# Performance work log

Hardware: AMD Instinct MI355X
Metric: run time of the kernel (lower is better)

Reference implementation:

```python
import jax, jax.numpy as jnp
import numpy as np

N1, N2 = 8192, 8192
E1, E2 = 131072, 131072
F_IN, NH, B = 64, 128, 256
D6 = 6 * NH  # set2set in_channels = 768


def _gcn(x, W, b, src, dst, ew, n):
    xw = x @ W
    loop = jnp.arange(n)
    s = jnp.concatenate([src, loop])
    d = jnp.concatenate([dst, loop])
    w = jnp.concatenate([ew, jnp.ones((n,), ew.dtype)])
    deg = jax.ops.segment_sum(w, d, num_segments=n)
    dinv = jnp.where(deg > 0, jax.lax.rsqrt(deg), 0.0)
    norm = (dinv[s] * w * dinv[d])[:, None]
    return jax.ops.segment_sum(xw[s] * norm, d, num_segments=n) + b


def _leaky(x):
    return jax.nn.leaky_relu(x, 0.2)


def _l2norm(x):
    return x / jnp.maximum(jnp.linalg.norm(x, axis=1, keepdims=True), 1e-12)


def _set2set(x, batch, nseg, Wih, Whh, bih, bhh, steps=2):
    # Set2Set pooling: LSTM(input=2d, hidden=d) + segment softmax attention
    d = x.shape[1]
    h = jnp.zeros((nseg, d), x.dtype)
    c = jnp.zeros((nseg, d), x.dtype)
    q_star = jnp.zeros((nseg, 2 * d), x.dtype)
    for _ in range(steps):
        gates = q_star @ Wih.T + h @ Whh.T + bih + bhh
        gi, gf, gg, go = jnp.split(gates, 4, axis=1)  # torch LSTM gate order i,f,g,o
        c = jax.nn.sigmoid(gf) * c + jax.nn.sigmoid(gi) * jnp.tanh(gg)
        h = jax.nn.sigmoid(go) * jnp.tanh(c)
        e = jnp.sum(x * h[batch], axis=1)
        emax = jax.ops.segment_max(e, batch, num_segments=nseg)
        ee = jnp.exp(e - emax[batch])
        a = ee / jax.ops.segment_sum(ee, batch, num_segments=nseg)[batch]
        r = jax.ops.segment_sum(a[:, None] * x, batch, num_segments=nseg)
        q_star = jnp.concatenate([h, r], axis=1)
    return q_star


def setup_inputs():
    key = jax.random.key(0)
    ks = jax.random.split(key, 20)
    f32 = jnp.float32

    def xav(k, shp):
        fan_in, fan_out = shp[-1], shp[0] if len(shp) == 2 else shp[-1]
        lim = float(np.sqrt(6.0 / (shp[0] + shp[1])))
        return jax.random.uniform(k, shp, f32, -lim, lim)

    inp = {}
    inp["features_1"] = jax.random.normal(ks[0], (N1, F_IN), f32)
    inp["features_2"] = jax.random.normal(ks[1], (N2, F_IN), f32)
    inp["edge_attr_1"] = jax.random.uniform(ks[2], (E1,), f32)
    inp["edge_attr_2"] = jax.random.uniform(ks[3], (E2,), f32)
    inp["W0"] = xav(ks[4], (F_IN, NH)); inp["b0"] = jnp.zeros((NH,), f32)
    inp["W1"] = xav(ks[5], (NH, NH)); inp["b1"] = jnp.zeros((NH,), f32)
    inp["W2"] = xav(ks[6], (NH, NH)); inp["b2"] = jnp.zeros((NH,), f32)
    inp["Wih"] = xav(ks[7], (4 * D6, 2 * D6)); inp["bih"] = jnp.zeros((4 * D6,), f32)
    inp["Whh"] = xav(ks[8], (4 * D6, D6)); inp["bhh"] = jnp.zeros((4 * D6,), f32)
    inp["Wp1"] = xav(ks[9], (256, 4 * D6)); inp["bp1"] = jnp.zeros((256,), f32)
    inp["Wp2"] = xav(ks[10], (128, 256)); inp["bp2"] = jnp.zeros((128,), f32)
    inp["Wp3"] = xav(ks[11], (1, 128)); inp["bp3"] = jnp.zeros((1,), f32)
    inp["edge_index_1"] = jax.random.randint(ks[12], (2, E1), 0, N1)
    inp["edge_index_2"] = jax.random.randint(ks[13], (2, E2), 0, N2)
    inp["batch_1"] = jnp.sort(jax.random.randint(ks[14], (N1,), 0, B))
    inp["batch_2"] = jnp.sort(jax.random.randint(ks[15], (N2,), 0, B))
    return inp


def reference(features_1, features_2, edge_attr_1, edge_attr_2,
              W0, b0, W1, b1, W2, b2, Wih, bih, Whh, bhh,
              Wp1, bp1, Wp2, bp2, Wp3, bp3,
              edge_index_1, edge_index_2, batch_1, batch_2):
    s1, d1 = edge_index_1[0], edge_index_1[1]
    s2, d2 = edge_index_2[0], edge_index_2[1]

    f1a = _leaky(_gcn(features_1, W0, b0, s1, d1, edge_attr_1, N1))
    f2a = _leaky(_gcn(features_2, W0, b0, s2, d2, edge_attr_2, N2))
    f1b = _leaky(_gcn(f1a, W1, b1, s1, d1, edge_attr_1, N1))
    f2b = _leaky(_gcn(f2a, W1, b1, s2, d2, edge_attr_2, N2))
    f1c = _leaky(_gcn(f1b, W2, b2, s1, d1, edge_attr_1, N1))
    f2c = _leaky(_gcn(f2b, W2, b2, s2, d2, edge_attr_2, N2))
    h1 = jnp.concatenate([f1a, f1b, f1c], axis=1)  # [N1, 3*NH]
    h2 = jnp.concatenate([f2a, f2b, f2c], axis=1)  # [N2, 3*NH]

    # interaction: cosine-sim map masked to same-graph pairs (len_map)
    ns = _l2norm(h1)
    nv = _l2norm(h2)
    mask = (batch_1[:, None] == batch_2[None, :]).astype(ns.dtype)  # [N1, N2]
    imap = (ns @ nv.T) * mask
    f1 = jnp.concatenate([ns, imap @ nv], axis=1)      # [N1, 6*NH]
    f2 = jnp.concatenate([nv, imap.T @ ns], axis=1)    # [N2, 6*NH]

    g1 = _set2set(f1, batch_1, B, Wih, Whh, bih, bhh)  # [B, 12*NH]
    g2 = _set2set(f2, batch_2, B, Wih, Whh, bih, bhh)  # [B, 12*NH]
    z = jnp.concatenate([g1, g2], axis=1)              # [B, 24*NH]
    z = jax.nn.relu(z @ Wp1.T + bp1)
    z = jax.nn.relu(z @ Wp2.T + bp2)
    z = z @ Wp3.T + bp3
    return jax.nn.sigmoid(z).reshape(-1)
```

## Files before the change

### kernel.cpp

```cpp
#include <hip/hip_runtime.h>
#include <cmath>

#define N_NODES 8192
#define N_EDGES 131072
#define NB      256
#define NH      128
#define D3      384
#define D6      768
#define SMM     96
#define SLD     104
#define MAXDEG  64

typedef __attribute__((ext_vector_type(8))) short short8v;
typedef __attribute__((ext_vector_type(4))) float f32x4;
typedef unsigned short bf16t;

__device__ __forceinline__ float sigf(float x){ return 1.0f/(1.0f+__expf(-x)); }
__device__ __forceinline__ unsigned short f2bf(float x){
  unsigned u = __float_as_uint(x);
  unsigned r = u + 0x7FFF + ((u>>16)&1);
  return (unsigned short)(r>>16);
}
__device__ __forceinline__ float bfl(unsigned u){ return __uint_as_float(u<<16); }
__device__ __forceinline__ float bfh(unsigned u){ return __uint_as_float(u & 0xFFFF0000u); }
__device__ __forceinline__ float b2f(bf16t u){ return __uint_as_float(((unsigned)u)<<16); }
__device__ __forceinline__ float h0val(const float* bih, const float* bhh, int j){
  float c = sigf(bih[j]+bhh[j]) * tanhf(bih[2*D6+j]+bhh[2*D6+j]);
  return sigf(bih[3*D6+j]+bhh[3*D6+j]) * tanhf(c);
}

__device__ __forceinline__ void xw_body(int vb, int t,
    const bf16t* __restrict__ x1, const bf16t* __restrict__ x2, int xs, int K,
    const bf16t* __restrict__ Wt, bf16t* __restrict__ xw1, bf16t* __restrict__ xw2){
  int side = vb >> 8; int b = vb & 255;
  const bf16t* x = side? x2:x1;
  bf16t* xw = side? xw2:xw1;
  int w = t>>6, lane = t&63;
  int lm = lane&15, quad = lane>>4;
  int r0 = b*32 + (w>>1)*16;
  int c0 = (w&1)*64;
  const bf16t* a = x + (size_t)(r0+lm)*xs + quad*8;
  f32x4 acc[4] = {};
  for (int k=0;k<K;k+=32){
    short8v af = *(const short8v*)(a + k);
    #pragma unroll
    for (int ni=0;ni<4;ni++){
      short8v bf = *(const short8v*)(Wt + (size_t)(c0+ni*16+lm)*K + quad*8 + k);
      acc[ni] = __builtin_amdgcn_mfma_f32_16x16x32_bf16(af, bf, acc[ni], 0,0,0);
    }
  }
  #pragma unroll
  for (int ni=0;ni<4;ni++)
    #pragma unroll
    for (int r=0;r<4;r++){
      int row = r0 + quad*4 + r, col = c0 + ni*16 + lm;
      xw[(size_t)row*NH + col] = f2bf(acc[ni][r]);
    }
}


__global__ __launch_bounds__(256) void k_setup(
    const float* __restrict__ fe1, const float* __restrict__ fe2,
    short* __restrict__ xf1, short* __restrict__ xf2,
    const float* __restrict__ W0, const float* __restrict__ W1, const float* __restrict__ W2,
    bf16t* __restrict__ Wt,
    int* ecur1, int* ecur2, int* cnt1, int* cnt2){
  int b = blockIdx.x, tid = threadIdx.x;
  if (b < 1024){
    int t = b*256 + tid;
    int side = t >= 131072; int i = t & 131071;
    float4 v = ((const float4*)(side? fe2:fe1))[i];
    short4 o = { (short)f2bf(v.x), (short)f2bf(v.y), (short)f2bf(v.z), (short)f2bf(v.w) };
    ((short4*)(side? xf2:xf1))[i] = o;
  } else if (b < 1027){
    int l = b - 1024;
    const float* W = (l==0)? W0 : ((l==1)? W1 : W2);
    int K = (l==0)? 64 : 128;
    bf16t* dst = Wt + ((l==0)? 0 : ((l==1)? 128*64 : 128*64+128*128));
    for (int idx = tid; idx < 128*K; idx += 256){
      int n = idx / K, k = idx - n*K;
      dst[idx] = f2bf(W[k*NH + n]);
    }
  } else {
    int t = (b-1027)*256 + tid;
    if (t < N_NODES){ ecur1[t]=0; ecur2[t]=0; }
    if (t < NB){ cnt1[t]=0; cnt2[t]=0; }
  }
}

__global__ __launch_bounds__(256) void k_fill2(
    const int* __restrict__ ei1, const float* __restrict__ ea1,
    const int* __restrict__ ei2, const float* __restrict__ ea2,
    int* cur1, int* es1, float* ec1, int* cur2, int* es2, float* ec2,
    const int* __restrict__ b1, const int* __restrict__ b2, int* cnt1, int* cnt2,
    const bf16t* __restrict__ xf1, const bf16t* __restrict__ xf2,
    const bf16t* __restrict__ Wt, bf16t* __restrict__ xwA1, bf16t* __restrict__ xwA2){
  int blk = blockIdx.x;
  if (blk < 1024){
    int idx = blk*256 + threadIdx.x;
    int side = idx >= N_EDGES;
    int e = idx & (N_EDGES-1);
    const int* ei = side? ei2:ei1; const float* ea = side? ea2:ea1;
    int* cur = side? cur2:cur1; int* es = side? es2:es1; float* ec = side? ec2:ec1;
    int s = ei[e], d = ei[N_EDGES+e];
    int pos = atomicAdd(&cur[d], 1);
    if (pos < MAXDEG){
      es[d*MAXDEG + pos] = s;
      ec[d*MAXDEG + pos] = ea[e];
    }
    if (idx < N_NODES){ atomicAdd(&cnt1[b1[idx]],1); atomicAdd(&cnt2[b2[idx]],1); }
  } else {
    xw_body(blk-1024, threadIdx.x, xf1, xf2, 64, 64, Wt, xwA1, xwA2);
  }
}

__global__ __launch_bounds__(256) void k_deg2(
    const int* __restrict__ cur1, const float* __restrict__ ec1, float* deg1,
    const int* __restrict__ cur2, const float* __restrict__ ec2, float* deg2,
    const int* __restrict__ c1, const int* __restrict__ c2, int* st1, int* st2){
  __shared__ int ps[256];
  int blk = blockIdx.x, t = threadIdx.x;
  if (blk < 64){
    int idx = blk*256 + t;
    int side = idx >= N_NODES;
    int i = idx & (N_NODES-1);
    const int* cur = side? cur2:cur1;
    const float* ec = side? ec2:ec1;
    float* deg = side? deg2:deg1;
    int ce = cur[i]; if (ce > MAXDEG) ce = MAXDEG;
    float s = 1.0f;
    const float* p = ec + (size_t)i*MAXDEG;
    for (int k=0;k<ce;k++) s += p[k];
    deg[i] = s;
  } else {
    const int* c = (blk==65)? c2:c1; int* st = (blk==65)? st2:st1;
    ps[t]=c[t]; __syncthreads();
    for (int d=1; d<256; d<<=1){
      int v = (t>=d)? ps[t-d]:0;
      __syncthreads();
      ps[t]+=v;
      __syncthreads();
    }
    st[t+1]=ps[t];
    if (t==0) st[0]=0;
  }
}


__global__ __launch_bounds__(256) void k_gxw(
    const bf16t* __restrict__ xwi1, const bf16t* __restrict__ xwi2,
    const int* __restrict__ cur1, const int* __restrict__ cur2,
    const int* __restrict__ es1, const int* __restrict__ es2,
    float* __restrict__ ec1, float* __restrict__ ec2,
    const float* __restrict__ d1, const float* __restrict__ d2,
    const float* __restrict__ bias, int loff, int coefmode,
    bf16t* __restrict__ h1, bf16t* __restrict__ h2,
    const bf16t* __restrict__ Wl,
    bf16t* __restrict__ xwo1, bf16t* __restrict__ xwo2){
  int blk = blockIdx.x;
  int side = blk >> 9; int b = blk & 511;
  const ushort4* xw = (const ushort4*)(side? xwi2:xwi1);
  const int* cur = side? cur2:cur1;
  const int* es  = side? es2:es1;
  float* ec = side? ec2:ec1;
  const float* deg = side? d2:d1;
  bf16t* h = side? h2:h1;
  int t = threadIdx.x;
  int c4 = t & 31;
  float4 bv = ((const float4*)bias)[c4];
  #pragma unroll
  for (int grp=0; grp<2; grp++){
    int i = b*16 + grp*8 + (t>>5);
    float dgi = deg[i];
    float sc = 1.0f/dgi;
    float rsq_d = rsqrtf(dgi);
    ushort4 v = xw[(size_t)i*32 + c4];
    float4 acc = {b2f(v.x)*sc, b2f(v.y)*sc, b2f(v.z)*sc, b2f(v.w)*sc};
    int r = i*MAXDEG;
    int ce = cur[i]; if (ce > MAXDEG) ce = MAXDEG;
    int r1 = r + ce;
    for (; r+3<r1; r+=4){
      int s0=es[r], s1=es[r+1], s2=es[r+2], s3=es[r+3];
      float w0=ec[r], w1=ec[r+1], w2=ec[r+2], w3=ec[r+3];
      if (coefmode){
        w0 *= rsqrtf(deg[s0])*rsq_d;
        w1 *= rsqrtf(deg[s1])*rsq_d;
        w2 *= rsqrtf(deg[s2])*rsq_d;
        w3 *= rsqrtf(deg[s3])*rsq_d;
        if (c4==0){ ec[r]=w0; ec[r+1]=w1; ec[r+2]=w2; ec[r+3]=w3; }
      }
      ushort4 u0 = xw[(size_t)s0*32 + c4];
      ushort4 u1 = xw[(size_t)s1*32 + c4];
      ushort4 u2 = xw[(size_t)s2*32 + c4];
      ushort4 u3 = xw[(size_t)s3*32 + c4];
      acc.x += b2f(u0.x)*w0 + b2f(u1.x)*w1 + b2f(u2.x)*w2 + b2f(u3.x)*w3;
      acc.y += b2f(u0.y)*w0 + b2f(u1.y)*w1 + b2f(u2.y)*w2 + b2f(u3.y)*w3;
      acc.z += b2f(u0.z)*w0 + b2f(u1.z)*w1 + b2f(u2.z)*w2 + b2f(u3.z)*w3;
      acc.w += b2f(u0.w)*w0 + b2f(u1.w)*w1 + b2f(u2.w)*w2 + b2f(u3.w)*w3;
    }
    for (; r<r1; r++){
      int s0=es[r]; float w0=ec[r];
      if (coefmode){
        w0 *= rsqrtf(deg[s0])*rsq_d;
        if (c4==0) ec[r]=w0;
      }
      ushort4 u0 = xw[(size_t)s0*32 + c4];
      acc.x+=b2f(u0.x)*w0; acc.y+=b2f(u0.y)*w0; acc.z+=b2f(u0.z)*w0; acc.w+=b2f(u0.w)*w0;
    }
    acc.x+=bv.x; acc.y+=bv.y; acc.z+=bv.z; acc.w+=bv.w;
    acc.x = (acc.x>0.f)?acc.x:0.2f*acc.x;
    acc.y = (acc.y>0.f)?acc.y:0.2f*acc.y;
    acc.z = (acc.z>0.f)?acc.z:0.2f*acc.z;
    acc.w = (acc.w>0.f)?acc.w:0.2f*acc.w;
    ((ushort4*)(h + (size_t)i*D3 + loff))[c4] =
      make_ushort4(f2bf(acc.x), f2bf(acc.y), f2bf(acc.z), f2bf(acc.w));
  }
  __syncthreads();
  int w = t>>6, lane = t&63;
  int lm = lane&15, quad = lane>>4;
  const bf16t* x = (side? h2:h1) + loff;
  int r0 = b*16;
  int c0 = w*32;
  const bf16t* a = x + (size_t)(r0+lm)*D3 + quad*8;
  bf16t* xwo = side? xwo2:xwo1;
  f32x4 acc0={0,0,0,0}, acc1={0,0,0,0};
  for (int k=0;k<128;k+=32){
    short8v af = *(const short8v*)(a + k);
    short8v b0 = *(const short8v*)(Wl + (size_t)(c0+lm)*128 + quad*8 + k);
    short8v b1 = *(const short8v*)(Wl + (size_t)(c0+16+lm)*128 + quad*8 + k);
    acc0 = __builtin_amdgcn_mfma_f32_16x16x32_bf16(af, b0, acc0, 0,0,0);
    acc1 = __builtin_amdgcn_mfma_f32_16x16x32_bf16(af, b1, acc1, 0,0,0);
  }
  #pragma unroll
  for (int r=0;r<4;r++){
    int row = r0 + quad*4 + r;
    xwo[(size_t)row*NH + c0 + lm]      = f2bf(acc0[r]);
    xwo[(size_t)row*NH + c0 + 16 + lm] = f2bf(acc1[r]);
  }
}

__global__ __launch_bounds__(256) void k_gather(const bf16t* __restrict__ xw1, const bf16t* __restrict__ xw2,
                                                const int* __restrict__ cur1, const int* __restrict__ cur2,
                                                const int* __restrict__ es1, const int* __restrict__ es2,
                                                const float* __restrict__ ec1, const float* __restrict__ ec2,
                                                const float* __restrict__ d1, const float* __restrict__ d2,
                                                const float* __restrict__ b,
                                                bf16t* __restrict__ h1, bf16t* __restrict__ h2, int loff,
                                                int l2mode, bf16t* __restrict__ f1, bf16t* __restrict__ f2,
                                                const float* __restrict__ Wih, short* __restrict__ Wih16,
                                                const float* __restrict__ Wp1, short* __restrict__ Wp116,
                                                const float* __restrict__ Whh,
                                                const float* __restrict__ bih, const float* __restrict__ bhh,
                                                float* __restrict__ cvec){
  __shared__ float hs_cv[D6];
  int blk = blockIdx.x;
  int t = threadIdx.x;
  if (blk >= 2048){
    if (blk < 4352){
      int tt = (blk-2048)*256 + t;
      int n = tt/192, q = tt - n*192;
      float4 v = ((const float4*)(Wih + (size_t)n*1536 + 768))[q];
      short4 o = { (short)f2bf(v.x), (short)f2bf(v.y), (short)f2bf(v.z), (short)f2bf(v.w) };
      ((short4*)Wih16)[tt] = o;
    } else if (blk < 5120){
      int tt = (blk-4352)*256 + t;
      float4 v = ((const float4*)Wp1)[tt];
      short4 o = { (short)f2bf(v.x), (short)f2bf(v.y), (short)f2bf(v.z), (short)f2bf(v.w) };
      ((short4*)Wp116)[tt] = o;
    } else {
      int j0 = (blk - 5120)*4;
      for (int k=t; k<D6; k+=256) hs_cv[k] = h0val(bih,bhh,k);
      __syncthreads();
      int w = t>>6, lane = t&63;
      int j = j0 + w;
      const float4* wi = (const float4*)(Wih + (size_t)j*(2*D6));
      const float4* wh = (const float4*)(Whh + (size_t)j*D6);
      const float4* h4 = (const float4*)hs_cv;
      float acc=0;
      #pragma unroll
      for (int m=0;m<3;m++){
        float4 hv = h4[m*64+lane];
        float4 a = wi[m*64+lane];
        float4 bb = wh[m*64+lane];
        acc += hv.x*(a.x+bb.x) + hv.y*(a.y+bb.y) + hv.z*(a.z+bb.z) + hv.w*(a.w+bb.w);
      }
      #pragma unroll
      for (int m=1;m<64;m<<=1) acc += __shfl_xor(acc,m,64);
      if (lane==0) cvec[j]=acc+bih[j]+bhh[j];
    }
    return;
  }
  int side = blk >> 10; int bb = blk & 1023;
  const ushort4* xw = (const ushort4*)(side? xw2:xw1);
  const int* cur = side? cur2:cur1;
  const int* es  = side? es2:es1;
  const float* ec= side? ec2:ec1;
  const float* deg = side? d2:d1;
  bf16t* h = side? h2:h1;
  int i = bb*8 + (t>>5);
  int c4 = t & 31;
  float sc = 1.0f/deg[i];
  ushort4 v = xw[(size_t)i*32 + c4];
  float4 acc = {b2f(v.x)*sc, b2f(v.y)*sc, b2f(v.z)*sc, b2f(v.w)*sc};
  int r = i*MAXDEG;
  int ce = cur[i]; if (ce > MAXDEG) ce = MAXDEG;
  int r1 = r + ce;
  for (; r+3<r1; r+=4){
    int s0=es[r], s1=es[r+1], s2=es[r+2], s3=es[r+3];
    float w0=ec[r], w1=ec[r+1], w2=ec[r+2], w3=ec[r+3];
    ushort4 u0 = xw[(size_t)s0*32 + c4];
    ushort4 u1 = xw[(size_t)s1*32 + c4];
    ushort4 u2 = xw[(size_t)s2*32 + c4];
    ushort4 u3 = xw[(size_t)s3*32 + c4];
    acc.x += b2f(u0.x)*w0 + b2f(u1.x)*w1 + b2f(u2.x)*w2 + b2f(u3.x)*w3;
    acc.y += b2f(u0.y)*w0 + b2f(u1.y)*w1 + b2f(u2.y)*w2 + b2f(u3.y)*w3;
    acc.z += b2f(u0.z)*w0 + b2f(u1.z)*w1 + b2f(u2.z)*w2 + b2f(u3.z)*w3;
    acc.w += b2f(u0.w)*w0 + b2f(u1.w)*w1 + b2f(u2.w)*w2 + b2f(u3.w)*w3;
  }
  for (; r<r1; r++){
    int s0=es[r]; float w0=ec[r];
    ushort4 u0 = xw[(size_t)s0*32 + c4];
    acc.x+=b2f(u0.x)*w0; acc.y+=b2f(u0.y)*w0; acc.z+=b2f(u0.z)*w0; acc.w+=b2f(u0.w)*w0;
  }
  float4 bv = ((const float4*)b)[c4];
  acc.x+=bv.x; acc.y+=bv.y; acc.z+=bv.z; acc.w+=bv.w;
  acc.x = (acc.x>0.f)?acc.x:0.2f*acc.x;
  acc.y = (acc.y>0.f)?acc.y:0.2f*acc.y;
  acc.z = (acc.z>0.f)?acc.z:0.2f*acc.z;
  acc.w = (acc.w>0.f)?acc.w:0.2f*acc.w;
  if (!l2mode){
    ((ushort4*)(h + (size_t)i*D3 + loff))[c4] =
      make_ushort4(f2bf(acc.x), f2bf(acc.y), f2bf(acc.z), f2bf(acc.w));
  } else {
    ushort4 u0 = ((const ushort4*)(h + (size_t)i*D3))[c4];
    ushort4 u1 = ((const ushort4*)(h + (size_t)i*D3 + 128))[c4];
    float4 v0 = {b2f(u0.x), b2f(u0.y), b2f(u0.z), b2f(u0.w)};
    float4 v1 = {b2f(u1.x), b2f(u1.y), b2f(u1.z), b2f(u1.w)};
    float ss = v0.x*v0.x+v0.y*v0.y+v0.z*v0.z+v0.w*v0.w
             + v1.x*v1.x+v1.y*v1.y+v1.z*v1.z+v1.w*v1.w
             + acc.x*acc.x+acc.y*acc.y+acc.z*acc.z+acc.w*acc.w;
    #pragma unroll
    for (int m=1;m<32;m<<=1) ss += __shfl_xor(ss, m, 64);
    float scale = 1.0f/fmaxf(sqrtf(ss), 1e-12f);
    bf16t* f = side? f2:f1;
    ((ushort4*)(f + (size_t)i*D6))[c4]       = make_ushort4(f2bf(v0.x*scale),f2bf(v0.y*scale),f2bf(v0.z*scale),f2bf(v0.w*scale));
    ((ushort4*)(f + (size_t)i*D6 + 128))[c4] = make_ushort4(f2bf(v1.x*scale),f2bf(v1.y*scale),f2bf(v1.z*scale),f2bf(v1.w*scale));
    ((ushort4*)(f + (size_t)i*D6 + 256))[c4] = make_ushort4(f2bf(acc.x*scale),f2bf(acc.y*scale),f2bf(acc.z*scale),f2bf(acc.w*scale));
  }
}

__global__ __launch_bounds__(256) void k_inter(bf16t* __restrict__ f1, bf16t* __restrict__ f2,
                                               const int* __restrict__ st1, const int* __restrict__ st2,
                                               const float* __restrict__ bih, const float* __restrict__ bhh,
                                               bf16t* __restrict__ Ab){
  __shared__ __align__(16) bf16t Sld[SMM*SLD];
  int bx = blockIdx.x;
  int t = threadIdx.x;
  int side = bx >> 8, g = bx & (NB-1);
  int i0 = st1[g]; int n1 = st1[g+1]-i0; if (n1>SMM) n1=SMM;
  int j0 = st2[g]; int n2 = st2[g+1]-j0; if (n2>SMM) n2=SMM;
  int cnt = side? n2 : n1;
  int J   = side? n1 : n2;
  int r0base = side? j0 : i0;
  int c0base = side? i0 : j0;
  const bf16t* rowp = (side? f2 : f1);
  const bf16t* colp = (side? f1 : f2);
  const bf16t* src = colp + (size_t)c0base*D6;
  bf16t* dst = (side? f2 : f1) + (size_t)r0base*D6 + D3;
  int w = t>>6, lane = t&63;
  int lm = lane & 15, quad = lane >> 4;
  int nti = (cnt+15)>>4, ntj = (J+15)>>4;
  for (int tile = w; tile < nti*ntj; tile += 4){
    int ti = tile/ntj, tj = tile - ti*ntj;
    int ar = r0base + ti*16 + lm; if (ar > N_NODES-1) ar = N_NODES-1;
    int br = c0base + tj*16 + lm; if (br > N_NODES-1) br = N_NODES-1;
    const bf16t* a = rowp + (size_t)ar*D6 + quad*8;
    const bf16t* b = colp + (size_t)br*D6 + quad*8;
    f32x4 acc = {0,0,0,0};
    #pragma unroll
    for (int k=0; k<384; k+=32){
      short8v af = *(const short8v*)(a + k);
      short8v bf = *(const short8v*)(b + k);
      acc = __builtin_amdgcn_mfma_f32_16x16x32_bf16(af, bf, acc, 0, 0, 0);
    }
    int col = tj*16 + lm;
    #pragma unroll
    for (int r=0;r<4;r++){
      int row = ti*16 + quad*4 + r;
      if (row < cnt && col < J)
        Sld[row*SLD + col] = f2bf(acc[r]);
    }
  }
  __syncthreads();
  for (int row = w; row < cnt; row += 4){
    float acc[6] = {};
    const bf16t* sr = Sld + row*SLD;
    for (int j = 0; j < J; j++){
      float s = b2f(sr[j]);
      const uint* xr = (const uint*)(src + (size_t)j*D6);
      #pragma unroll
      for (int m=0;m<3;m++){
        uint rv = xr[m*64+lane];
        acc[m*2+0] += s*bfl(rv);
        acc[m*2+1] += s*bfh(rv);
      }
    }
    #pragma unroll
    for (int m=0;m<3;m++)
      ((ushort2*)(dst + (size_t)row*D6 + m*128))[lane] =
        make_ushort2(f2bf(acc[m*2]), f2bf(acc[m*2+1]));
  }
  __syncthreads();
  {
    float4* hs = (float4*)Sld;
    float* e_s = ((float*)Sld) + 768;
    float* part = ((float*)Sld) + 864;
    const bf16t* x = rowp + (size_t)r0base*D6;
    if (t<192){
      int j = t*4;
      hs[t] = make_float4(h0val(bih,bhh,j), h0val(bih,bhh,j+1), h0val(bih,bhh,j+2), h0val(bih,bhh,j+3));
    }
    __syncthreads();
    for (int n=w; n<cnt; n+=4){
      const uint2* xr = (const uint2*)(x + (size_t)n*D6);
      float p = 0;
      #pragma unroll
      for (int m=0;m<3;m++){
        uint2 rv = xr[m*64+lane];
        float4 hvv = hs[m*64+lane];
        p += bfl(rv.x)*hvv.x + bfh(rv.x)*hvv.y + bfl(rv.y)*hvv.z + bfh(rv.y)*hvv.w;
      }
      #pragma unroll
      for (int m=1;m<64;m<<=1) p += __shfl_xor(p,m,64);
      if (lane==0) e_s[n]=p;
    }
    __syncthreads();
    if (w==0){
      float mx=-INFINITY;
      for (int n=lane;n<cnt;n+=64) mx=fmaxf(mx,e_s[n]);
      #pragma unroll
      for (int m=1;m<64;m<<=1) mx=fmaxf(mx,__shfl_xor(mx,m,64));
      float s=0;
      for (int n=lane;n<cnt;n+=64) s+=__expf(e_s[n]-mx);
      #pragma unroll
      for (int m=1;m<64;m<<=1) s+=__shfl_xor(s,m,64);
      float inv=1.0f/s;
      for (int n=lane;n<cnt;n+=64) e_s[n]=__expf(e_s[n]-mx)*inv;
    }
    __syncthreads();
    float av[3][4] = {};
    for (int n=w; n<cnt; n+=4){
      float a = e_s[n];
      const uint2* xr = (const uint2*)(x + (size_t)n*D6);
      #pragma unroll
      for (int m=0;m<3;m++){
        uint2 rv = xr[m*64+lane];
        av[m][0]+=a*bfl(rv.x); av[m][1]+=a*bfh(rv.x); av[m][2]+=a*bfl(rv.y); av[m][3]+=a*bfh(rv.y);
      }
    }
    #pragma unroll
    for (int m=0;m<3;m++)
      *(float4*)&part[w*D6 + (m*64+lane)*4] = make_float4(av[m][0],av[m][1],av[m][2],av[m][3]);
    __syncthreads();
    if (t<192){
      float4 p0 = *(const float4*)&part[0*D6 + t*4];
      float4 p1 = *(const float4*)&part[1*D6 + t*4];
      float4 p2 = *(const float4*)&part[2*D6 + t*4];
      float4 p3 = *(const float4*)&part[3*D6 + t*4];
      float4 s = make_float4(p0.x+p1.x+p2.x+p3.x, p0.y+p1.y+p2.y+p3.y,
                             p0.z+p1.z+p2.z+p3.z, p0.w+p1.w+p2.w+p3.w);
      ushort4 o = make_ushort4(f2bf(s.x), f2bf(s.y), f2bf(s.z), f2bf(s.w));
      ((ushort4*)(Ab + (size_t)(side*NB+g)*D6))[t]=o;
    }
  }
}


__global__ __launch_bounds__(256) void k_att(const bf16t* __restrict__ f1, const bf16t* __restrict__ f2,
                                             const float* __restrict__ hbase, int perseg,
                                             const float* __restrict__ bih, const float* __restrict__ bhh,
                                             const int* __restrict__ st1, const int* __restrict__ st2,
                                             bf16t* __restrict__ dst16, long sidestep, long dstride){
  __shared__ float4 hs[192];
  __shared__ float e_s[SMM];
  __shared__ float part[4][D6];
  int side = blockIdx.x >> 8, g = blockIdx.x & (NB-1);
  const int* st = side? st2:st1;
  int n0 = st[g]; int cnt = st[g+1]-n0; if (cnt>SMM) cnt=SMM;
  const bf16t* x = (side? f2:f1) + (size_t)n0*D6;
  int t = threadIdx.x, w = t>>6, lane = t&63;
  if (t<192){
    if (perseg){
      hs[t] = ((const float4*)(hbase + (size_t)(side*NB+g)*D6))[t];
    } else {
      int j = t*4;
      hs[t] = make_float4(h0val(bih,bhh,j), h0val(bih,bhh,j+1), h0val(bih,bhh,j+2), h0val(bih,bhh,j+3));
    }
  }
  __syncthreads();
  for (int n=w; n<cnt; n+=4){
    const uint2* xr = (const uint2*)(x + (size_t)n*D6);
    float p = 0;
    #pragma unroll
    for (int m=0;m<3;m++){
      uint2 rv = xr[m*64+lane];
      float4 hvv = hs[m*64+lane];
      p += bfl(rv.x)*hvv.x + bfh(rv.x)*hvv.y + bfl(rv.y)*hvv.z + bfh(rv.y)*hvv.w;
    }
    #pragma unroll
    for (int m=1;m<64;m<<=1) p += __shfl_xor(p,m,64);
    if (lane==0) e_s[n]=p;
  }
  __syncthreads();
  if (w==0){
    float mx=-INFINITY;
    for (int n=lane;n<cnt;n+=64) mx=fmaxf(mx,e_s[n]);
    #pragma unroll
    for (int m=1;m<64;m<<=1) mx=fmaxf(mx,__shfl_xor(mx,m,64));
    float s=0;
    for (int n=lane;n<cnt;n+=64) s+=__expf(e_s[n]-mx);
    #pragma unroll
    for (int m=1;m<64;m<<=1) s+=__shfl_xor(s,m,64);
    float inv=1.0f/s;
    for (int n=lane;n<cnt;n+=64) e_s[n]=__expf(e_s[n]-mx)*inv;
  }
  __syncthreads();
  float av[3][4] = {};
  for (int n=w; n<cnt; n+=4){
    float a = e_s[n];
    const uint2* xr = (const uint2*)(x + (size_t)n*D6);
    #pragma unroll
    for (int m=0;m<3;m++){
      uint2 rv = xr[m*64+lane];
      av[m][0]+=a*bfl(rv.x); av[m][1]+=a*bfh(rv.x); av[m][2]+=a*bfl(rv.y); av[m][3]+=a*bfh(rv.y);
    }
  }
  #pragma unroll
  for (int m=0;m<3;m++)
    *(float4*)&part[w][(m*64+lane)*4] = make_float4(av[m][0],av[m][1],av[m][2],av[m][3]);
  __syncthreads();
  if (t<192){
    float4 p0 = *(const float4*)&part[0][t*4];
    float4 p1 = *(const float4*)&part[1][t*4];
    float4 p2 = *(const float4*)&part[2][t*4];
    float4 p3 = *(const float4*)&part[3][t*4];
    float4 s = make_float4(p0.x+p1.x+p2.x+p3.x, p0.y+p1.y+p2.y+p3.y,
                           p0.z+p1.z+p2.z+p3.z, p0.w+p1.w+p2.w+p3.w);
    ushort4 o = make_ushort4(f2bf(s.x), f2bf(s.y), f2bf(s.z), f2bf(s.w));
    ushort4* dp = (ushort4*)(dst16 + side*sidestep + (size_t)g*dstride);
    dp[t]=o;
  }
}

__global__ __launch_bounds__(256) void k_gates(const short* __restrict__ A16,
                                               const short* __restrict__ B16,
                                               const float* __restrict__ cvec,
                                               const float* __restrict__ bih, const float* __restrict__ bhh,
                                               float* __restrict__ h1s, bf16t* __restrict__ z16){
  __shared__ float gbuf[4][16][66];
  int w = threadIdx.x >> 6, lane = threadIdx.x & 63;
  int lm = lane & 15, quad = lane >> 4;
  int bm = blockIdx.x * 16;
  int jb = blockIdx.y * 64;
  const short* a = A16 + (size_t)(bm + lm)*768 + quad*8;
  const short* b = B16 + (size_t)(w*768 + jb + lm)*768 + quad*8;
  f32x4 acc0={0,0,0,0}, acc1={0,0,0,0}, acc2={0,0,0,0}, acc3={0,0,0,0};
  for (int k=0; k<768; k+=32){
    short8v af = *(const short8v*)(a + k);
    short8v b0 = *(const short8v*)(b + k);
    short8v b1 = *(const short8v*)(b + 16*768 + k);
    short8v b2 = *(const short8v*)(b + 32*768 + k);
    short8v b3 = *(const short8v*)(b + 48*768 + k);
    acc0 = __builtin_amdgcn_mfma_f32_16x16x32_bf16(af, b0, acc0, 0, 0, 0);
    acc1 = __builtin_amdgcn_mfma_f32_16x16x32_bf16(af, b1, acc1, 0, 0, 0);
    acc2 = __builtin_amdgcn_mfma_f32_16x16x32_bf16(af, b2, acc2, 0, 0, 0);
    acc3 = __builtin_amdgcn_mfma_f32_16x16x32_bf16(af, b3, acc3, 0, 0, 0);
  }
  #pragma unroll
  for (int r=0;r<4;r++){
    gbuf[w][quad*4+r][lm]      = acc0[r];
    gbuf[w][quad*4+r][16+lm]   = acc1[r];
    gbuf[w][quad*4+r][32+lm]   = acc2[r];
    gbuf[w][quad*4+r][48+lm]   = acc3[r];
  }
  __syncthreads();
  int t = threadIdx.x;
  #pragma unroll
  for (int u=0; u<4; u++){
    int p = t + u*256;
    int mm = p>>6, jj = p&63;
    int j = jb + jj, m = bm + mm;
    float g4[4];
    #pragma unroll
    for (int q=0;q<4;q++) g4[q] = gbuf[q][mm][jj] + cvec[q*D6 + j];
    float c0j = sigf(bih[j]+bhh[j]) * tanhf(bih[2*D6+j]+bhh[2*D6+j]);
    float c = sigf(g4[1])*c0j + sigf(g4[0])*tanhf(g4[2]);
    float h = sigf(g4[3])*tanhf(c);
    h1s[(size_t)m*D6 + j] = h;
    int side = m>>8, g = m&255;
    z16[(size_t)g*3072 + side*1536 + j] = f2bf(h);
  }
}

__global__ __launch_bounds__(256) void k_gemm_mfma_p1(const short* __restrict__ A16,
                                                      const short* __restrict__ B16,
                                                      float* __restrict__ pout){
  int w = threadIdx.x >> 6, lane = threadIdx.x & 63;
  int lm = lane & 15, quad = lane >> 4;
  int bm = blockIdx.x * 16;
  int bn = w * 64;
  int kbase = blockIdx.y * 192;
  const short* a = A16 + (size_t)(bm + lm)*3072 + quad*8 + kbase;
  const short* b = B16 + (size_t)(bn + lm)*3072 + quad*8 + kbase;
  f32x4 acc0={0,0,0,0}, acc1={0,0,0,0}, acc2={0,0,0,0}, acc3={0,0,0,0};
  for (int k=0; k<192; k+=32){
    short8v af = *(const short8v*)(a + k);
    short8v b0 = *(const short8v*)(b + k);
    short8v b1 = *(const short8v*)(b + 16*3072 + k);
    short8v b2 = *(const short8v*)(b + 32*3072 + k);
    short8v b3 = *(const short8v*)(b + 48*3072 + k);
    acc0 = __builtin_amdgcn_mfma_f32_16x16x32_bf16(af, b0, acc0, 0, 0, 0);
    acc1 = __builtin_amdgcn_mfma_f32_16x16x32_bf16(af, b1, acc1, 0, 0, 0);
    acc2 = __builtin_amdgcn_mfma_f32_16x16x32_bf16(af, b2, acc2, 0, 0, 0);
    acc3 = __builtin_amdgcn_mfma_f32_16x16x32_bf16(af, b3, acc3, 0, 0, 0);
  }
  float* po = pout + (size_t)blockIdx.y*256*256;
  #pragma unroll
  for (int r=0;r<4;r++){
    size_t base = (size_t)(bm + quad*4 + r)*256 + bn + lm;
    po[base]      = acc0[r];
    po[base + 16] = acc1[r];
    po[base + 32] = acc2[r];
    po[base + 48] = acc3[r];
  }
}

__global__ __launch_bounds__(128) void k_p23(const float* __restrict__ pbuf, const float* __restrict__ bp1,
                                             const float* __restrict__ Wp2, const float* __restrict__ bp2,
                                             const float* __restrict__ Wp3, const float* __restrict__ bp3,
                                             float* __restrict__ out){
  __shared__ float zr[256];
  __shared__ float ws[2];
  int m = blockIdx.x, t = threadIdx.x;
  float2 zacc = ((const float2*)(bp1))[t];
  #pragma unroll
  for (int p=0;p<16;p++){
    float2 v = ((const float2*)(pbuf + (size_t)p*256*256 + (size_t)m*256))[t];
    zacc.x += v.x; zacc.y += v.y;
  }
  zr[2*t]   = fmaxf(zacc.x, 0.f);
  zr[2*t+1] = fmaxf(zacc.y, 0.f);
  __syncthreads();
  const float4* wrow = (const float4*)(Wp2 + (size_t)t*256);
  const float4* z4 = (const float4*)zr;
  float acc = bp2[t];
  #pragma unroll 8
  for (int k=0;k<64;k++){
    float4 wv = wrow[k], zv = z4[k];
    acc += wv.x*zv.x + wv.y*zv.y + wv.z*zv.z + wv.w*zv.w;
  }
  float p = fmaxf(acc,0.f)*Wp3[t];
  #pragma unroll
  for (int o=32;o;o>>=1) p += __shfl_down(p,o,64);
  if ((t&63)==0) ws[t>>6]=p;
  __syncthreads();
  if (t==0){ float v=ws[0]+ws[1]+bp3[0]; out[m]=1.0f/(1.0f+__expf(-v)); }
}


extern "C" void kernel_launch(void* const* d_in, const int* in_sizes, int n_in,
                              void* d_out, int out_size, void* d_ws, size_t ws_size,
                              hipStream_t stream){
  const float* feat1=(const float*)d_in[0];
  const float* feat2=(const float*)d_in[1];
  const float* ea1  =(const float*)d_in[2];
  const float* ea2  =(const float*)d_in[3];
  const float* W0=(const float*)d_in[4];  const float* b0=(const float*)d_in[5];
  const float* W1=(const float*)d_in[6];  const float* b1=(const float*)d_in[7];
  const float* W2=(const float*)d_in[8];  const float* b2=(const float*)d_in[9];
  const float* Wih=(const float*)d_in[10]; const float* bih=(const float*)d_in[11];
  const float* Whh=(const float*)d_in[12]; const float* bhh=(const float*)d_in[13];
  const float* Wp1=(const float*)d_in[14]; const float* bp1=(const float*)d_in[15];
  const float* Wp2=(const float*)d_in[16]; const float* bp2=(const float*)d_in[17];
  const float* Wp3=(const float*)d_in[18]; const float* bp3=(const float*)d_in[19];
  const int* ei1=(const int*)d_in[20]; const int* ei2=(const int*)d_in[21];
  const int* batch1=(const int*)d_in[22]; const int* batch2=(const int*)d_in[23];
  float* out = (float*)d_out;

  float* base = (float*)d_ws;
  size_t off = 0;
  auto alloc = [&](size_t n)->float* { float* r = base + off; off += (n + 255) & ~(size_t)255; return r; };
  float* deg1 = alloc(N_NODES);          float* deg2 = alloc(N_NODES);
  bf16t* xwA1 = (bf16t*)alloc((size_t)N_NODES*NH/2);
  bf16t* xwA2 = (bf16t*)alloc((size_t)N_NODES*NH/2);
  bf16t* xwB1 = (bf16t*)alloc((size_t)N_NODES*NH/2);
  bf16t* xwB2 = (bf16t*)alloc((size_t)N_NODES*NH/2);
  bf16t* hb1  = (bf16t*)alloc((size_t)N_NODES*D3/2);
  bf16t* hb2  = (bf16t*)alloc((size_t)N_NODES*D3/2);
  bf16t* xf1  = (bf16t*)alloc((size_t)N_NODES*64/2);
  bf16t* xf2  = (bf16t*)alloc((size_t)N_NODES*64/2);
  bf16t* Wtb  = (bf16t*)alloc((size_t)(128*64 + 2*128*128)/2);
  bf16t* f1   = (bf16t*)alloc((size_t)N_NODES*D6/2);
  bf16t* f2   = (bf16t*)alloc((size_t)N_NODES*D6/2);
  float* ecoef1 = alloc((size_t)N_NODES*MAXDEG);  float* ecoef2 = alloc((size_t)N_NODES*MAXDEG);
  float* cvec = alloc(4*D6);
  float* h1s  = alloc((size_t)512*D6);
  bf16t* zbuf16 = (bf16t*)alloc((size_t)256*3072/2);
  float* pbuf = alloc((size_t)16*256*256);
  short* Abuf16 = (short*)alloc((size_t)512*D6/2);
  short* Wih16  = (short*)alloc((size_t)3072*D6/2);
  short* Wp116  = (short*)alloc((size_t)256*3072/2);
  int* cnt1 = (int*)alloc(NB);   int* cnt2 = (int*)alloc(NB);
  int* st1  = (int*)alloc(NB+1); int* st2  = (int*)alloc(NB+1);
  int* ecur1= (int*)alloc(N_NODES); int* ecur2 = (int*)alloc(N_NODES);
  int* esrc1= (int*)alloc((size_t)N_NODES*MAXDEG); int* esrc2 = (int*)alloc((size_t)N_NODES*MAXDEG);
  (void)ws_size; (void)in_sizes; (void)n_in; (void)out_size;

  k_setup  <<<1059,256,0,stream>>>(feat1,feat2,(short*)xf1,(short*)xf2,
                                   W0,W1,W2,Wtb, ecur1,ecur2,cnt1,cnt2);
  k_fill2  <<<1536,256,0,stream>>>(ei1,ea1, ei2,ea2,
                                   ecur1,esrc1,ecoef1, ecur2,esrc2,ecoef2,
                                   batch1,batch2,cnt1,cnt2,
                                   xf1,xf2,Wtb,xwA1,xwA2);
  k_deg2   <<<66,256,0,stream>>>(ecur1,ecoef1,deg1, ecur2,ecoef2,deg2,
                                 cnt1,cnt2,st1,st2);

  const bf16t* Wt1 = Wtb + 128*64;
  const bf16t* Wt2 = Wtb + 128*64 + 128*128;
  k_gxw<<<1024,256,0,stream>>>(xwA1,xwA2, ecur1,ecur2, esrc1,esrc2, ecoef1,ecoef2,
                               deg1,deg2, b0, 0, 1, hb1,hb2, Wt1, xwB1,xwB2);
  k_gxw<<<1024,256,0,stream>>>(xwB1,xwB2, ecur1,ecur2, esrc1,esrc2, ecoef1,ecoef2,
                               deg1,deg2, b1, NH, 0, hb1,hb2, Wt2, xwA1,xwA2);
  k_gather <<<5888,256,0,stream>>>(xwA1,xwA2,ecur1,ecur2,esrc1,esrc2,ecoef1,ecoef2,
                                   deg1,deg2,b2,hb1,hb2,2*NH,1,f1,f2,
                                   Wih,(short*)Wih16, Wp1,(short*)Wp116,
                                   Whh,bih,bhh,cvec);

  k_inter <<<512,256,0,stream>>>(f1,f2,st1,st2,bih,bhh,(bf16t*)Abuf16);

  k_gates<<<dim3(32,12),256,0,stream>>>(Abuf16, Wih16, cvec, bih, bhh, h1s, zbuf16);

  k_att<<<512,256,0,stream>>>(f1,f2,h1s,1,bih,bhh,st1,st2,
                              zbuf16+768,(long)1536,(long)3072);

  k_gemm_mfma_p1<<<dim3(16,16),256,0,stream>>>((const short*)zbuf16, Wp116, pbuf);
  k_p23 <<<256,128,0,stream>>>(pbuf, bp1, Wp2, bp2, Wp3, bp3, out);
}
```

Before: 344.4 us.

## Move weight-conversion side work into k_inter and widen it to 512 threads

Moves the bf16 conversion of Wih and Wp1 and the cvec precompute out of k_gather and into extra blocks of k_inter. k_inter now runs 512-thread blocks (8 waves) instead of 256, so its tile, row and attention loops stride by 8 and the partial-sum reduction adds 8 slices. The aim is to shorten k_gather and spread the inter-graph work across more waves. The cost is larger shared memory per block (7008 floats), and the side work now runs alongside the heavier k_inter blocks.

```diff
diff --git a/kernel.cpp b/kernel.cpp
--- a/kernel.cpp
+++ b/kernel.cpp
@@ -246,50 +246,8 @@
                                                 const float* __restrict__ d1, const float* __restrict__ d2,
                                                 const float* __restrict__ b,
                                                 bf16t* __restrict__ h1, bf16t* __restrict__ h2, int loff,
-                                                int l2mode, bf16t* __restrict__ f1, bf16t* __restrict__ f2,
-                                                const float* __restrict__ Wih, short* __restrict__ Wih16,
-                                                const float* __restrict__ Wp1, short* __restrict__ Wp116,
-                                                const float* __restrict__ Whh,
-                                                const float* __restrict__ bih, const float* __restrict__ bhh,
-                                                float* __restrict__ cvec){
-  __shared__ float hs_cv[D6];
+                                                int l2mode, bf16t* __restrict__ f1, bf16t* __restrict__ f2){
   int blk = blockIdx.x;
-  int t = threadIdx.x;
-  if (blk >= 2048){
-    if (blk < 4352){
-      int tt = (blk-2048)*256 + t;
-      int n = tt/192, q = tt - n*192;
-      float4 v = ((const float4*)(Wih + (size_t)n*1536 + 768))[q];
-      short4 o = { (short)f2bf(v.x), (short)f2bf(v.y), (short)f2bf(v.z), (short)f2bf(v.w) };
-      ((short4*)Wih16)[tt] = o;
-    } else if (blk < 5120){
-      int tt = (blk-4352)*256 + t;
-      float4 v = ((const float4*)Wp1)[tt];
-      short4 o = { (short)f2bf(v.x), (short)f2bf(v.y), (short)f2bf(v.z), (short)f2bf(v.w) };
-      ((short4*)Wp116)[tt] = o;
-    } else {
-      int j0 = (blk - 5120)*4;
-      for (int k=t; k<D6; k+=256) hs_cv[k] = h0val(bih,bhh,k);
-      __syncthreads();
-      int w = t>>6, lane = t&63;
-      int j = j0 + w;
-      const float4* wi = (const float4*)(Wih + (size_t)j*(2*D6));
-      const float4* wh = (const float4*)(Whh + (size_t)j*D6);
-      const float4* h4 = (const float4*)hs_cv;
-      float acc=0;
-      #pragma unroll
-      for (int m=0;m<3;m++){
-        float4 hv = h4[m*64+lane];
-        float4 a = wi[m*64+lane];
-        float4 bb = wh[m*64+lane];
-        acc += hv.x*(a.x+bb.x) + hv.y*(a.y+bb.y) + hv.z*(a.z+bb.z) + hv.w*(a.w+bb.w);
-      }
-      #pragma unroll
-      for (int m=1;m<64;m<<=1) acc += __shfl_xor(acc,m,64);
-      if (lane==0) cvec[j]=acc+bih[j]+bhh[j];
-    }
-    return;
-  }
   int side = blk >> 10; int bb = blk & 1023;
   const ushort4* xw = (const ushort4*)(side? xw2:xw1);
   const int* cur = side? cur2:cur1;
@@ -297,6 +255,7 @@
   const float* ec= side? ec2:ec1;
   const float* deg = side? d2:d1;
   bf16t* h = side? h2:h1;
+  int t = threadIdx.x;
   int i = bb*8 + (t>>5);
   int c4 = t & 31;
   float sc = 1.0f/deg[i];
@@ -349,13 +308,52 @@
   }
 }
 
-__global__ __launch_bounds__(256) void k_inter(bf16t* __restrict__ f1, bf16t* __restrict__ f2,
+__global__ __launch_bounds__(512) void k_inter(bf16t* __restrict__ f1, bf16t* __restrict__ f2,
                                                const int* __restrict__ st1, const int* __restrict__ st2,
                                                const float* __restrict__ bih, const float* __restrict__ bhh,
-                                               bf16t* __restrict__ Ab){
-  __shared__ __align__(16) bf16t Sld[SMM*SLD];
+                                               bf16t* __restrict__ Ab,
+                                               const float* __restrict__ Wih, short* __restrict__ Wih16,
+                                               const float* __restrict__ Wp1, short* __restrict__ Wp116,
+                                               const float* __restrict__ Whh, float* __restrict__ cvec){
+  __shared__ __align__(16) float smem[7008];
+  bf16t* Sld = (bf16t*)smem;
   int bx = blockIdx.x;
   int t = threadIdx.x;
+  int w = t>>6, lane = t&63;
+  if (bx >= 512){
+    if (bx < 1664){
+      int tt = (bx-512)*512 + t;
+      int n = tt/192, q = tt - n*192;
+      float4 v = ((const float4*)(Wih + (size_t)n*1536 + 768))[q];
+      short4 o = { (short)f2bf(v.x), (short)f2bf(v.y), (short)f2bf(v.z), (short)f2bf(v.w) };
+      ((short4*)Wih16)[tt] = o;
+    } else if (bx < 2048){
+      int tt = (bx-1664)*512 + t;
+      float4 v = ((const float4*)Wp1)[tt];
+      short4 o = { (short)f2bf(v.x), (short)f2bf(v.y), (short)f2bf(v.z), (short)f2bf(v.w) };
+      ((short4*)Wp116)[tt] = o;
+    } else {
+      int j0 = (bx - 2048)*8;
+      for (int k=t; k<D6; k+=512) smem[k] = h0val(bih,bhh,k);
+      __syncthreads();
+      int j = j0 + w;
+      const float4* wi = (const float4*)(Wih + (size_t)j*(2*D6));
+      const float4* wh = (const float4*)(Whh + (size_t)j*D6);
+      const float4* h4 = (const float4*)smem;
+      float acc=0;
+      #pragma unroll
+      for (int m=0;m<3;m++){
+        float4 hv = h4[m*64+lane];
+        float4 a = wi[m*64+lane];
+        float4 bb = wh[m*64+lane];
+        acc += hv.x*(a.x+bb.x) + hv.y*(a.y+bb.y) + hv.z*(a.z+bb.z) + hv.w*(a.w+bb.w);
+      }
+      #pragma unroll
+      for (int m=1;m<64;m<<=1) acc += __shfl_xor(acc,m,64);
+      if (lane==0) cvec[j]=acc+bih[j]+bhh[j];
+    }
+    return;
+  }
   int side = bx >> 8, g = bx & (NB-1);
   int i0 = st1[g]; int n1 = st1[g+1]-i0; if (n1>SMM) n1=SMM;
   int j0 = st2[g]; int n2 = st2[g+1]-j0; if (n2>SMM) n2=SMM;
@@ -367,10 +365,9 @@
   const bf16t* colp = (side? f1 : f2);
   const bf16t* src = colp + (size_t)c0base*D6;
   bf16t* dst = (side? f2 : f1) + (size_t)r0base*D6 + D3;
-  int w = t>>6, lane = t&63;
   int lm = lane & 15, quad = lane >> 4;
   int nti = (cnt+15)>>4, ntj = (J+15)>>4;
-  for (int tile = w; tile < nti*ntj; tile += 4){
+  for (int tile = w; tile < nti*ntj; tile += 8){
     int ti = tile/ntj, tj = tile - ti*ntj;
     int ar = r0base + ti*16 + lm; if (ar > N_NODES-1) ar = N_NODES-1;
     int br = c0base + tj*16 + lm; if (br > N_NODES-1) br = N_NODES-1;
@@ -392,7 +389,7 @@
     }
   }
   __syncthreads();
-  for (int row = w; row < cnt; row += 4){
+  for (int row = w; row < cnt; row += 8){
     float acc[6] = {};
     const bf16t* sr = Sld + row*SLD;
     for (int j = 0; j < J; j++){
@@ -412,16 +409,16 @@
   }
   __syncthreads();
   {
-    float4* hs = (float4*)Sld;
-    float* e_s = ((float*)Sld) + 768;
-    float* part = ((float*)Sld) + 864;
+    float4* hs = (float4*)smem;
+    float* e_s = smem + 768;
+    float* part = smem + 864;
     const bf16t* x = rowp + (size_t)r0base*D6;
     if (t<192){
       int j = t*4;
       hs[t] = make_float4(h0val(bih,bhh,j), h0val(bih,bhh,j+1), h0val(bih,bhh,j+2), h0val(bih,bhh,j+3));
     }
     __syncthreads();
-    for (int n=w; n<cnt; n+=4){
+    for (int n=w; n<cnt; n+=8){
       const uint2* xr = (const uint2*)(x + (size_t)n*D6);
       float p = 0;
       #pragma unroll
@@ -449,7 +446,7 @@
     }
     __syncthreads();
     float av[3][4] = {};
-    for (int n=w; n<cnt; n+=4){
+    for (int n=w; n<cnt; n+=8){
       float a = e_s[n];
       const uint2* xr = (const uint2*)(x + (size_t)n*D6);
       #pragma unroll
@@ -463,12 +460,12 @@
       *(float4*)&part[w*D6 + (m*64+lane)*4] = make_float4(av[m][0],av[m][1],av[m][2],av[m][3]);
     __syncthreads();
     if (t<192){
-      float4 p0 = *(const float4*)&part[0*D6 + t*4];
-      float4 p1 = *(const float4*)&part[1*D6 + t*4];
-      float4 p2 = *(const float4*)&part[2*D6 + t*4];
-      float4 p3 = *(const float4*)&part[3*D6 + t*4];
-      float4 s = make_float4(p0.x+p1.x+p2.x+p3.x, p0.y+p1.y+p2.y+p3.y,
-                             p0.z+p1.z+p2.z+p3.z, p0.w+p1.w+p2.w+p3.w);
+      float4 s = make_float4(0.f,0.f,0.f,0.f);
+      #pragma unroll
+      for (int p8=0;p8<8;p8++){
+        float4 pv = *(const float4*)&part[p8*D6 + t*4];
+        s.x+=pv.x; s.y+=pv.y; s.z+=pv.z; s.w+=pv.w;
+      }
       ushort4 o = make_ushort4(f2bf(s.x), f2bf(s.y), f2bf(s.z), f2bf(s.w));
       ((ushort4*)(Ab + (size_t)(side*NB+g)*D6))[t]=o;
     }
@@ -731,12 +728,11 @@
                                deg1,deg2, b0, 0, 1, hb1,hb2, Wt1, xwB1,xwB2);
   k_gxw<<<1024,256,0,stream>>>(xwB1,xwB2, ecur1,ecur2, esrc1,esrc2, ecoef1,ecoef2,
                                deg1,deg2, b1, NH, 0, hb1,hb2, Wt2, xwA1,xwA2);
-  k_gather <<<5888,256,0,stream>>>(xwA1,xwA2,ecur1,ecur2,esrc1,esrc2,ecoef1,ecoef2,
-                                   deg1,deg2,b2,hb1,hb2,2*NH,1,f1,f2,
-                                   Wih,(short*)Wih16, Wp1,(short*)Wp116,
-                                   Whh,bih,bhh,cvec);
-
-  k_inter <<<512,256,0,stream>>>(f1,f2,st1,st2,bih,bhh,(bf16t*)Abuf16);
+  k_gather <<<2048,256,0,stream>>>(xwA1,xwA2,ecur1,ecur2,esrc1,esrc2,ecoef1,ecoef2,
+                                   deg1,deg2,b2,hb1,hb2,2*NH,1,f1,f2);
+
+  k_inter <<<2432,512,0,stream>>>(f1,f2,st1,st2,bih,bhh,(bf16t*)Abuf16,
+                                  Wih,(short*)Wih16, Wp1,(short*)Wp116, Whh,cvec);
 
   k_gates<<<dim3(32,12),256,0,stream>>>(Abuf16, Wih16, cvec, bih, bhh, h1s, zbuf16);
 
```

After: 328.6 us. 4.6% less time.
